# Kernel optimization log

Hardware: AMD Instinct MI355X
Metric: run time of the kernel (lower is better)

The kernel has to match this reference:

```python
import jax, jax.numpy as jnp
import numpy as np
from itertools import permutations

# Static problem sizes: L=5 qubits, q=2**(L+1)=64 features, |G|=5!=120, 20 actions
L = 5
Q = 2 ** (L + 1)          # 64
G = 120                   # 5!
HID = 128
NACT = 20
B, T = 32, 64


def _build_tables():
    perms = list(permutations(range(L)))
    pidx = {p: i for i, p in enumerate(perms)}
    # inverse_table[i] = index of p_i^{-1}
    inv = [pidx[tuple(np.argsort(p))] for p in perms]
    # cayley[i, j] = index of p_i * p_j  (perm_prod(pi,pj) = tuple(pi[k] for k in pj))
    cayley = np.array([[pidx[tuple(pi[k] for k in pj)] for pj in perms] for pi in perms])
    # Hm[u, g] = index of permutation u * g^{-1} applied to x for group term g
    Hm = cayley[:, inv]
    # Gmap[u, p] = g such that Hm[u, g] == p  (row-wise bijection)
    Gmap = np.empty_like(Hm)
    Gmap[np.arange(G)[:, None], Hm] = np.arange(G)[None, :]
    # feature-level index maps: x_permuted = x[..., featperm[p]] matches torch
    # reshape(b,t,2,..,2).permute(0,1,2, g+3).reshape
    base = np.arange(Q).reshape((2,) * (L + 1))
    featperm = np.stack([
        base.transpose((0,) + tuple(i + 1 for i in p)).reshape(-1) for p in perms
    ])
    # action cosets: action a=(q0,q1) collects all perms with (p[0],p[1])==a
    acts = list(permutations(range(L), 2))
    aidx = {a: i for i, a in enumerate(acts)}
    coset_id = np.array([aidx[(p[0], p[1])] for p in perms])
    coset_size = np.bincount(coset_id, minlength=len(acts)).astype(np.float32)
    return featperm, Gmap, coset_id, coset_size


FEATPERM, GMAP, COSET_ID, COSET_SIZE = _build_tables()


def setup_inputs() -> dict:
    key = jax.random.key(0)
    ks = jax.random.split(key, 7)
    s = (2.0 / HID) ** 0.5  # kaiming-ish scale
    return {
        "x": jax.random.normal(ks[0], (B, T, Q), jnp.float32),
        "eq_weight": jax.random.normal(ks[1], (G, Q, HID), jnp.float32) * s,
        "eq_bias": jax.random.uniform(ks[2], (G, HID), jnp.float32, -0.01, 0.01),
        "W1": jax.random.normal(ks[3], (HID, HID), jnp.float32) * s,
        "b1": jax.random.uniform(ks[4], (HID,), jnp.float32, -0.01, 0.01),
        "Wout": jax.random.normal(ks[5], (HID, NACT), jnp.float32) * s,
        "bout": jax.random.uniform(ks[6], (NACT,), jnp.float32, -0.01, 0.01),
    }


def reference(x, eq_weight, eq_bias, W1, b1, Wout, bout):
    featperm = jnp.asarray(FEATPERM)          # (G, Q) int
    gmap = jnp.asarray(GMAP)                  # (G, G) int
    coset_id = jnp.asarray(COSET_ID)          # (G,) int
    coset_size = jnp.asarray(COSET_SIZE)      # (NACT,) float

    # all qubit-level permutations of the input: (G, b, t, q)
    Xp = jnp.moveaxis(x[..., featperm], 2, 0)
    # Equivariant layer for ALL u at once:
    # result(u) = (1/G) * sum_p Xp[p] @ W[Gmap[u,p]] + mean_g bias[g]
    Wu = eq_weight[gmap]                      # (G_u, G_p, Q, HID)
    e = jnp.einsum('pbtq,upqh->ubth', Xp, Wu) / G + eq_bias.mean(0)
    h = jax.nn.relu(e)
    h = jax.nn.relu(h @ W1 + b1)              # second hidden layer (dropout_rate=0)
    out = h @ Wout + bout                     # (G, b, t, NACT)
    m = out.mean(-1)                          # (G, b, t)
    # y_i = mean over u in coset_i of m[u]
    y = jax.ops.segment_sum(m, coset_id, num_segments=NACT)
    y = y / coset_size[:, None, None]
    return jnp.transpose(y, (1, 2, 0))        # (b, t, NACT)
```

## Files before the change

### kernel.cpp

```cpp
#include <hip/hip_runtime.h>

typedef _Float16 f16;
typedef __attribute__((ext_vector_type(8))) _Float16 f16x8;
typedef __attribute__((ext_vector_type(4))) float f32x4;
typedef __attribute__((ext_vector_type(4))) unsigned int u32x4;
typedef __attribute__((ext_vector_type(8))) unsigned short ushort8;

#define QF   64
#define GG   120
#define HID  128
#define NACT 20
#define BTOT 2048

#define WEFF_OFF 0u
#define XH_OFF   1966080u
#define W1F_OFF  2490368u
#define MISC_OFF 2523136u
#define ABUF_OFF 2524224u

template <typename T>
__device__ __forceinline__ void keepv(T& v) { asm volatile("" : "+v"(v)); }

__device__ __forceinline__ unsigned idx_to_packed(int i) {
    unsigned avail = 0x43210u, pp = 0u;
    const int fct[4] = {24, 6, 2, 1};
#pragma unroll
    for (int k = 0; k < 4; ++k) {
        int d = i / fct[k]; i -= d * fct[k];
        pp |= ((avail >> (4 * d)) & 0xFu) << (4 * k);
        unsigned mask = (1u << (4 * d)) - 1u;
        avail = (avail & mask) | ((avail >> 4) & ~mask);
    }
    pp |= (avail & 0xFu) << 16;
    return pp;
}

__device__ __forceinline__ int packed_to_idx(unsigned pp) {
    const int fct[4] = {24, 6, 2, 1};
    int idx = 0;
#pragma unroll
    for (int k = 0; k < 4; ++k) {
        unsigned pk = (pp >> (4 * k)) & 0xFu;
        int c = 0;
#pragma unroll
        for (int j = k + 1; j < 5; ++j)
            c += (int)(((pp >> (4 * j)) & 0xFu) < pk);
        idx += c * fct[k];
    }
    return idx;
}

__device__ __forceinline__ unsigned compose_packed(unsigned pa, unsigned pb) {
    unsigned pc = 0;
#pragma unroll
    for (int k = 0; k < 5; ++k) {
        unsigned bk = (pb >> (4 * k)) & 0xFu;
        pc |= ((pa >> (4 * bk)) & 0xFu) << (4 * k);
    }
    return pc;
}

__device__ __forceinline__ unsigned invert_packed(unsigned pp) {
    unsigned pi = 0;
#pragma unroll
    for (int k = 0; k < 5; ++k)
        pi |= (unsigned)k << (4 * ((pp >> (4 * k)) & 0xFu));
    return pi;
}

__device__ __forceinline__ unsigned s4_packed(int i) {
    unsigned avail = 0x3210u, pp = 0u;
    const int f3[3] = {6, 2, 1};
#pragma unroll
    for (int k = 0; k < 3; ++k) {
        int d = i / f3[k]; i -= d * f3[k];
        pp |= ((avail >> (4 * d)) & 0xFu) << (4 * k);
        unsigned mask = (1u << (4 * d)) - 1u;
        avail = (avail & mask) | ((avail >> 4) & ~mask);
    }
    pp |= (avail & 0xFu) << 12;
    pp |= 4u << 16;
    return pp;
}

__device__ __forceinline__ unsigned crep_pp(int t) {
    unsigned pp = 0x43210u;
    pp &= ~(0xFu << (4 * t));
    pp &= ~(0xFu << 16);
    pp |= 4u << (4 * t);
    pp |= (unsigned)t << 16;
    return pp;
}

__device__ __forceinline__ int bitperm_r(unsigned ppi, int r) {
    int val = r & 32;
#pragma unroll
    for (int k = 0; k < 5; ++k) {
        int pik = (ppi >> (4 * k)) & 0xF;
        val |= ((r >> (4 - pik)) & 1) << (4 - k);
    }
    return val;
}

__device__ __forceinline__ int coset_member(int a, int e) {
    int i = a >> 2, jj = a & 3;
    int j = jj + (jj >= i ? 1 : 0);
    unsigned mask = 0x1Fu & ~(1u << i) & ~(1u << j);
    int d0 = __builtin_ctz(mask); mask &= mask - 1u;
    int d1 = __builtin_ctz(mask); mask &= mask - 1u;
    int d2 = __builtin_ctz(mask);
    int k0 = e >> 1;
    int p2 = k0 == 0 ? d0 : (k0 == 1 ? d1 : d2);
    int r0 = k0 == 0 ? d1 : d0;
    int r1 = k0 == 2 ? d1 : d2;
    int p3 = (e & 1) ? r1 : r0;
    int p4 = (e & 1) ? r0 : r1;
    unsigned pp = (unsigned)i | ((unsigned)j << 4) | ((unsigned)p2 << 8)
                | ((unsigned)p3 << 12) | ((unsigned)p4 << 16);
    return packed_to_idx(pp);
}

__device__ __forceinline__ unsigned short f2h(float f) {
    f16 h = (f16)f;
    return __builtin_bit_cast(unsigned short, h);
}
__device__ __forceinline__ unsigned pk2(float a, float b) {
    return (unsigned)f2h(a) | ((unsigned)f2h(b) << 16);
}

__global__ void prep_stage1(const float* __restrict__ x, const float* __restrict__ W1,
                            const float* __restrict__ eq_bias, const float* __restrict__ Wout,
                            const float* __restrict__ bout, const float* __restrict__ eqw,
                            float* __restrict__ misc,
                            unsigned short* __restrict__ xh,
                            unsigned short* __restrict__ w1f, float* __restrict__ Acan) {
    __shared__ int sg[24];
    __shared__ int sq[24][8];
    int b = blockIdx.x, t = threadIdx.x;
    if (b < 40) {
        int c = b >> 3, rbase = (b & 7) * 8;
        if (t < 24) sg[t] = packed_to_idx(compose_packed(s4_packed(t), crep_pp(c)));
        if (t < 192) {
            int si = t >> 3;
            sq[si][t & 7] = bitperm_r(invert_packed(s4_packed(si)), rbase + (t & 7));
        }
        __syncthreads();
        int h4 = (t & 31) * 4, rslot = t >> 5;
        f32x4 acc = {0.f, 0.f, 0.f, 0.f};
#pragma unroll
        for (int si = 0; si < 24; ++si) {
            f32x4 v = *(const f32x4*)(eqw + (unsigned)(sg[si] * QF + sq[si][rslot]) * HID + h4);
            acc = acc + v;
        }
        *(f32x4*)(Acan + (unsigned)(c * QF + rbase + rslot) * HID + h4) = acc;
    } else if (b < 552) {
        int idx = (b - 40) * 256 + t;
        xh[idx] = f2h(x[idx]);
    } else if (b < 560) {
        int idx = (b - 552) * 256 + t;
        int fg = idx >> 6, lane = idx & 63;
        int nt = fg >> 2, ks = fg & 3;
        int n = nt * 16 + (lane & 15), kg = lane >> 4;
        ushort8 v;
#pragma unroll
        for (int j = 0; j < 8; ++j) {
            int h = ks * 32 + ((j >> 2) << 4) + (kg << 2) + (j & 3);
            v[j] = f2h(W1[h * HID + n]);
        }
        *(ushort8*)(w1f + idx * 8) = v;
    } else {
        if (t < HID) {
            float s = 0.f;
            for (int g = 0; g < GG; ++g) s += eq_bias[g * HID + t];
            misc[t] = s * (1.f / GG);
            float wv = 0.f;
            for (int n = 0; n < NACT; ++n) wv += Wout[t * NACT + n];
            misc[HID + t] = wv * (1.f / NACT);
            if (t == 0) {
                float c = 0.f;
                for (int n = 0; n < NACT; ++n) c += bout[n];
                misc[2 * HID] = c * (1.f / NACT);
            }
        }
    }
}

__global__ void weff_stage2(const float* __restrict__ Acan,
                            unsigned short* __restrict__ weff) {
    __shared__ float Wacc[HID][QF + 1];
    __shared__ int rp[5][64];
    int u = blockIdx.x, t = threadIdx.x;
    unsigned upk = idx_to_packed(u);
    for (int i = t; i < 5 * 64; i += 256)
        rp[i >> 6][i & 63] = bitperm_r(compose_packed(upk, crep_pp(i >> 6)), i & 63);
    __syncthreads();
    int h = t & 127, qg = t >> 7;
    for (int i = 0; i < 32; ++i) {
        int q = qg * 32 + i;
        float s = 0.f;
#pragma unroll
        for (int c = 0; c < 5; ++c)
            s += Acan[(unsigned)(c * QF + rp[c][q]) * HID + h];
        Wacc[h][q] = s * (1.f / GG);
    }
    __syncthreads();
    for (int e = t; e < 1024; e += 256) {
        int fg = e >> 6, lane = e & 63;
        int hm = fg >> 1, ks = fg & 1;
        int hh = hm * 16 + (lane & 15), q0 = ks * 32 + (lane >> 4) * 8;
        ushort8 v;
#pragma unroll
        for (int j = 0; j < 8; ++j) v[j] = f2h(Wacc[hh][q0 + j]);
        *(ushort8*)(weff + (unsigned)(u * 16 + fg) * 64 * 8 + lane * 8) = v;
    }
}

__device__ __forceinline__ f32x4 mfma16(f16x8 a, f16x8 b, f32x4 c) {
    return __builtin_amdgcn_mfma_f32_16x16x32_f16(a, b, c, 0, 0, 0);
}

__global__ __launch_bounds__(128, 2)
void mlp_mfma(const unsigned short* __restrict__ xh,
              const unsigned short* __restrict__ weff,
              const unsigned short* __restrict__ w1f,
              const float* __restrict__ b1,
              const float* __restrict__ misc,
              float* __restrict__ out) {
    __shared__ __align__(16) unsigned short w1s[16384];
    __shared__ __align__(16) unsigned short wefs[8192];
    __shared__ float miscs[2 * HID];
    __shared__ float b1s[HID];

    int bid0 = blockIdx.x;
    int bid = (bid0 & 7) * 80 + (bid0 >> 3);
    int tile = bid & 31, a = bid >> 5;
    int rowbase = tile * 64;
    int t = threadIdx.x;
    int w = t >> 6, lane = t & 63;
    int lm = lane & 15, kg = lane >> 4;
    int xbase = rowbase + w * 32;

    int u0 = coset_member(a, 0);
#pragma unroll
    for (int i = 0; i < 16; ++i)
        *(u32x4*)(w1s + (i * 128 + t) * 8) = *(const u32x4*)(w1f + (i * 128 + t) * 8);
#pragma unroll
    for (int i = 0; i < 8; ++i)
        *(u32x4*)(wefs + (i * 128 + t) * 8) =
            *(const u32x4*)(weff + (unsigned)u0 * 8192 + (i * 128 + t) * 8);
    miscs[t] = misc[t];
    miscs[128 + t] = misc[128 + t];
    b1s[t] = b1[t];
    float cb = misc[2 * HID];

    f16x8 xb[2][2];
#pragma unroll
    for (int xt = 0; xt < 2; ++xt)
#pragma unroll
        for (int ks = 0; ks < 2; ++ks) {
            int off = (xbase + xt * 16 + lm) * QF + ks * 32 + kg * 8;
            xb[xt][ks] = *(const f16x8*)(xh + off);
            keepv(xb[xt][ks]);
        }
    __syncthreads();

    float macc[2][4];
#pragma unroll
    for (int xt = 0; xt < 2; ++xt)
#pragma unroll
        for (int r = 0; r < 4; ++r) macc[xt][r] = 0.f;

#pragma unroll 1
    for (int ui = 0; ui < 6; ++ui) {
        bool hasNext = (ui < 5);
        u32x4 pf[8];
        if (hasNext) {
            int un = coset_member(a, ui + 1);
            const unsigned short* wsrc = weff + (unsigned)un * 8192;
#pragma unroll
            for (int i = 0; i < 8; ++i)
                pf[i] = *(const u32x4*)(wsrc + (i * 128 + t) * 8);
        }

        f32x4 acc[2][8];
#pragma unroll
        for (int xt = 0; xt < 2; ++xt)
#pragma unroll
            for (int hm = 0; hm < 8; ++hm) acc[xt][hm] = (f32x4){0.f, 0.f, 0.f, 0.f};
#pragma unroll
        for (int hm = 0; hm < 8; ++hm)
#pragma unroll
            for (int ks = 0; ks < 2; ++ks) {
                f16x8 wf = *(const f16x8*)(wefs + ((hm * 2 + ks) * 64 + lane) * 8);
#pragma unroll
                for (int xt = 0; xt < 2; ++xt)
                    acc[xt][hm] = mfma16(wf, xb[xt][ks], acc[xt][hm]);
            }

        __syncthreads();
        if (hasNext) {
#pragma unroll
            for (int i = 0; i < 8; ++i)
                *(u32x4*)(wefs + (i * 128 + t) * 8) = pf[i];
        }

        f32x4 acc2[2][8];
#pragma unroll
        for (int xt = 0; xt < 2; ++xt)
#pragma unroll
            for (int nt = 0; nt < 8; ++nt) acc2[xt][nt] = (f32x4){0.f, 0.f, 0.f, 0.f};
#pragma unroll
        for (int ks = 0; ks < 4; ++ks) {
            f32x4 bm0 = *(const f32x4*)(miscs + (2 * ks) * 16 + kg * 4);
            f32x4 bm1 = *(const f32x4*)(miscs + (2 * ks + 1) * 16 + kg * 4);
            f16x8 pa[2];
#pragma unroll
            for (int xt = 0; xt < 2; ++xt) {
                f32x4 e0 = acc[xt][2 * ks] + bm0;
                f32x4 e1 = acc[xt][2 * ks + 1] + bm1;
#pragma unroll
                for (int r = 0; r < 4; ++r) {
                    e0[r] = e0[r] > 0.f ? e0[r] : 0.f;
                    e1[r] = e1[r] > 0.f ? e1[r] : 0.f;
                }
                u32x4 ph = {pk2(e0[0], e0[1]), pk2(e0[2], e0[3]),
                            pk2(e1[0], e1[1]), pk2(e1[2], e1[3])};
                pa[xt] = __builtin_bit_cast(f16x8, ph);
            }
#pragma unroll
            for (int nt = 0; nt < 8; ++nt) {
                f16x8 wb = *(const f16x8*)(w1s + ((nt * 4 + ks) * 64 + lane) * 8);
#pragma unroll
                for (int xt = 0; xt < 2; ++xt)
                    acc2[xt][nt] = mfma16(pa[xt], wb, acc2[xt][nt]);
            }
        }

#pragma unroll
        for (int nt = 0; nt < 8; ++nt) {
            float bb = b1s[nt * 16 + lm];
            float wm = miscs[HID + nt * 16 + lm];
#pragma unroll
            for (int xt = 0; xt < 2; ++xt)
#pragma unroll
                for (int r = 0; r < 4; ++r) {
                    float v = acc2[xt][nt][r] + bb;
                    v = v > 0.f ? v : 0.f;
                    macc[xt][r] += v * wm;
                }
        }
        __syncthreads();
    }

#pragma unroll
    for (int off = 1; off < 16; off <<= 1)
#pragma unroll
        for (int xt = 0; xt < 2; ++xt)
#pragma unroll
            for (int r = 0; r < 4; ++r)
                macc[xt][r] += __shfl_xor(macc[xt][r], off, 64);
    if (lm == 0) {
#pragma unroll
        for (int xt = 0; xt < 2; ++xt)
#pragma unroll
            for (int r = 0; r < 4; ++r)
                out[(unsigned)(xbase + xt * 16 + kg * 4 + r) * NACT + a] =
                    macc[xt][r] * (1.f / 6.f) + cb;
    }
}

extern "C" void kernel_launch(void* const* d_in, const int* in_sizes, int n_in,
                              void* d_out, int out_size, void* d_ws, size_t ws_size,
                              hipStream_t stream) {
    const float* x       = (const float*)d_in[0];
    const float* eqw     = (const float*)d_in[1];
    const float* eq_bias = (const float*)d_in[2];
    const float* W1      = (const float*)d_in[3];
    const float* b1      = (const float*)d_in[4];
    const float* Wout    = (const float*)d_in[5];
    const float* bout    = (const float*)d_in[6];
    float* out           = (float*)d_out;

    char* ws = (char*)d_ws;
    unsigned short* weff = (unsigned short*)(ws + WEFF_OFF);
    unsigned short* xhb  = (unsigned short*)(ws + XH_OFF);
    unsigned short* w1f  = (unsigned short*)(ws + W1F_OFF);
    float* misc   = (float*)(ws + MISC_OFF);
    float* Acan   = (float*)(ws + ABUF_OFF);

    hipLaunchKernelGGL(prep_stage1, dim3(561), dim3(256), 0, stream,
                       x, W1, eq_bias, Wout, bout, eqw, misc, xhb, w1f, Acan);
    hipLaunchKernelGGL(weff_stage2, dim3(120), dim3(256), 0, stream,
                       Acan, weff);
    hipLaunchKernelGGL(mlp_mfma, dim3(640), dim3(128), 0, stream,
                       xhb, weff, w1f, b1, misc, out);
}
```

Before: 41.29 us.

## Halve rows per block, double grid, read W1 fragments from global instead of LDS

Each wave now handles 16 rows instead of 32, so the grid doubles to 1280 blocks of 64 rows split as 32 per block. The 32 KB W1 staging in shared memory is removed and W1 fragments are loaded straight from global memory (cached) inside the second GEMM. This cuts LDS use and registers so more blocks can be resident and the tail is smaller. The cost is that the per-coset effective weights are fetched twice as often across blocks and W1 loads now go through the L1/L2 path, not LDS.

Result: faster. 40.19 us (-2.7%).

```diff
diff --git a/kernel.cpp b/kernel.cpp
--- a/kernel.cpp
+++ b/kernel.cpp
@@ -226,24 +226,20 @@
               const float* __restrict__ b1,
               const float* __restrict__ misc,
               float* __restrict__ out) {
-    __shared__ __align__(16) unsigned short w1s[16384];
     __shared__ __align__(16) unsigned short wefs[8192];
     __shared__ float miscs[2 * HID];
     __shared__ float b1s[HID];
 
     int bid0 = blockIdx.x;
-    int bid = (bid0 & 7) * 80 + (bid0 >> 3);
-    int tile = bid & 31, a = bid >> 5;
-    int rowbase = tile * 64;
+    int bid = (bid0 & 7) * 160 + (bid0 >> 3);
+    int tile = bid & 63, a = bid >> 6;
+    int rowbase = tile * 32;
     int t = threadIdx.x;
     int w = t >> 6, lane = t & 63;
     int lm = lane & 15, kg = lane >> 4;
-    int xbase = rowbase + w * 32;
+    int xbase = rowbase + w * 16;
 
     int u0 = coset_member(a, 0);
-#pragma unroll
-    for (int i = 0; i < 16; ++i)
-        *(u32x4*)(w1s + (i * 128 + t) * 8) = *(const u32x4*)(w1f + (i * 128 + t) * 8);
 #pragma unroll
     for (int i = 0; i < 8; ++i)
         *(u32x4*)(wefs + (i * 128 + t) * 8) =
@@ -253,22 +249,16 @@
     b1s[t] = b1[t];
     float cb = misc[2 * HID];
 
-    f16x8 xb[2][2];
-#pragma unroll
-    for (int xt = 0; xt < 2; ++xt)
-#pragma unroll
-        for (int ks = 0; ks < 2; ++ks) {
-            int off = (xbase + xt * 16 + lm) * QF + ks * 32 + kg * 8;
-            xb[xt][ks] = *(const f16x8*)(xh + off);
-            keepv(xb[xt][ks]);
-        }
+    f16x8 xb[2];
+#pragma unroll
+    for (int ks = 0; ks < 2; ++ks) {
+        int off = (xbase + lm) * QF + ks * 32 + kg * 8;
+        xb[ks] = *(const f16x8*)(xh + off);
+        keepv(xb[ks]);
+    }
     __syncthreads();
 
-    float macc[2][4];
-#pragma unroll
-    for (int xt = 0; xt < 2; ++xt)
-#pragma unroll
-        for (int r = 0; r < 4; ++r) macc[xt][r] = 0.f;
+    float macc[4] = {0.f, 0.f, 0.f, 0.f};
 
 #pragma unroll 1
     for (int ui = 0; ui < 6; ++ui) {
@@ -282,19 +272,15 @@
                 pf[i] = *(const u32x4*)(wsrc + (i * 128 + t) * 8);
         }
 
-        f32x4 acc[2][8];
-#pragma unroll
-        for (int xt = 0; xt < 2; ++xt)
-#pragma unroll
-            for (int hm = 0; hm < 8; ++hm) acc[xt][hm] = (f32x4){0.f, 0.f, 0.f, 0.f};
+        f32x4 acc[8];
+#pragma unroll
+        for (int hm = 0; hm < 8; ++hm) acc[hm] = (f32x4){0.f, 0.f, 0.f, 0.f};
 #pragma unroll
         for (int hm = 0; hm < 8; ++hm)
 #pragma unroll
             for (int ks = 0; ks < 2; ++ks) {
                 f16x8 wf = *(const f16x8*)(wefs + ((hm * 2 + ks) * 64 + lane) * 8);
-#pragma unroll
-                for (int xt = 0; xt < 2; ++xt)
-                    acc[xt][hm] = mfma16(wf, xb[xt][ks], acc[xt][hm]);
+                acc[hm] = mfma16(wf, xb[ks], acc[hm]);
             }
 
         __syncthreads();
@@ -304,35 +290,27 @@
                 *(u32x4*)(wefs + (i * 128 + t) * 8) = pf[i];
         }
 
-        f32x4 acc2[2][8];
-#pragma unroll
-        for (int xt = 0; xt < 2; ++xt)
-#pragma unroll
-            for (int nt = 0; nt < 8; ++nt) acc2[xt][nt] = (f32x4){0.f, 0.f, 0.f, 0.f};
+        f32x4 acc2[8];
+#pragma unroll
+        for (int nt = 0; nt < 8; ++nt) acc2[nt] = (f32x4){0.f, 0.f, 0.f, 0.f};
 #pragma unroll
         for (int ks = 0; ks < 4; ++ks) {
             f32x4 bm0 = *(const f32x4*)(miscs + (2 * ks) * 16 + kg * 4);
             f32x4 bm1 = *(const f32x4*)(miscs + (2 * ks + 1) * 16 + kg * 4);
-            f16x8 pa[2];
-#pragma unroll
-            for (int xt = 0; xt < 2; ++xt) {
-                f32x4 e0 = acc[xt][2 * ks] + bm0;
-                f32x4 e1 = acc[xt][2 * ks + 1] + bm1;
-#pragma unroll
-                for (int r = 0; r < 4; ++r) {
-                    e0[r] = e0[r] > 0.f ? e0[r] : 0.f;
-                    e1[r] = e1[r] > 0.f ? e1[r] : 0.f;
-                }
-                u32x4 ph = {pk2(e0[0], e0[1]), pk2(e0[2], e0[3]),
-                            pk2(e1[0], e1[1]), pk2(e1[2], e1[3])};
-                pa[xt] = __builtin_bit_cast(f16x8, ph);
-            }
+            f32x4 e0 = acc[2 * ks] + bm0;
+            f32x4 e1 = acc[2 * ks + 1] + bm1;
+#pragma unroll
+            for (int r = 0; r < 4; ++r) {
+                e0[r] = e0[r] > 0.f ? e0[r] : 0.f;
+                e1[r] = e1[r] > 0.f ? e1[r] : 0.f;
+            }
+            u32x4 ph = {pk2(e0[0], e0[1]), pk2(e0[2], e0[3]),
+                        pk2(e1[0], e1[1]), pk2(e1[2], e1[3])};
+            f16x8 pa = __builtin_bit_cast(f16x8, ph);
 #pragma unroll
             for (int nt = 0; nt < 8; ++nt) {
-                f16x8 wb = *(const f16x8*)(w1s + ((nt * 4 + ks) * 64 + lane) * 8);
-#pragma unroll
-                for (int xt = 0; xt < 2; ++xt)
-                    acc2[xt][nt] = mfma16(pa[xt], wb, acc2[xt][nt]);
+                f16x8 wb = *(const f16x8*)(w1f + ((nt * 4 + ks) * 64 + lane) * 8);
+                acc2[nt] = mfma16(pa, wb, acc2[nt]);
             }
         }
 
@@ -341,13 +319,11 @@
             float bb = b1s[nt * 16 + lm];
             float wm = miscs[HID + nt * 16 + lm];
 #pragma unroll
-            for (int xt = 0; xt < 2; ++xt)
-#pragma unroll
-                for (int r = 0; r < 4; ++r) {
-                    float v = acc2[xt][nt][r] + bb;
-                    v = v > 0.f ? v : 0.f;
-                    macc[xt][r] += v * wm;
-                }
+            for (int r = 0; r < 4; ++r) {
+                float v = acc2[nt][r] + bb;
+                v = v > 0.f ? v : 0.f;
+                macc[r] += v * wm;
+            }
         }
         __syncthreads();
     }
@@ -355,17 +331,13 @@
 #pragma unroll
     for (int off = 1; off < 16; off <<= 1)
 #pragma unroll
-        for (int xt = 0; xt < 2; ++xt)
-#pragma unroll
-            for (int r = 0; r < 4; ++r)
-                macc[xt][r] += __shfl_xor(macc[xt][r], off, 64);
+        for (int r = 0; r < 4; ++r)
+            macc[r] += __shfl_xor(macc[r], off, 64);
     if (lm == 0) {
 #pragma unroll
-        for (int xt = 0; xt < 2; ++xt)
-#pragma unroll
-            for (int r = 0; r < 4; ++r)
-                out[(unsigned)(xbase + xt * 16 + kg * 4 + r) * NACT + a] =
-                    macc[xt][r] * (1.f / 6.f) + cb;
+        for (int r = 0; r < 4; ++r)
+            out[(unsigned)(xbase + kg * 4 + r) * NACT + a] =
+                macc[r] * (1.f / 6.f) + cb;
     }
 }
 
@@ -392,6 +364,6 @@
                        x, W1, eq_bias, Wout, bout, eqw, misc, xhb, w1f, Acan);
     hipLaunchKernelGGL(weff_stage2, dim3(120), dim3(256), 0, stream,
                        Acan, weff);
-    hipLaunchKernelGGL(mlp_mfma, dim3(640), dim3(128), 0, stream,
+    hipLaunchKernelGGL(mlp_mfma, dim3(1280), dim3(128), 0, stream,
                        xhb, weff, w1f, b1, misc, out);
 }
```
